# Performance work log

Measured on AMD Instinct MI355X. Metric: run time of the kernel, lower is better.

The kernel has to match this reference:

```python
import jax, jax.numpy as jnp
import numpy as np

MOMENTUM = 0.99
EPS = 1e-08


def setup_inputs() -> dict:
    key = jax.random.key(0)
    k1, = jax.random.split(key, 1)
    B, F, T = 32, 257, 3000
    mag = jax.random.uniform(k1, (B, F, T), dtype=jnp.float32)  # magnitudes >= 0
    bias = jnp.zeros((1,), dtype=jnp.float32)
    running_mean = jnp.ones((1,), dtype=jnp.float32)
    return {"mag": mag, "bias": bias, "running_mean": running_mean}


def reference(mag, bias, running_mean):
    """Causal per-frame EMA energy normalization (eval-mode sequence path).

    mag: [B, F, T] -> (mag_norm [B, F, T], mag_mean [B, 1, T])
    """
    B, F, T = mag.shape
    frame_means = mag.mean(axis=1)          # [B, T]
    init = jnp.broadcast_to(running_mean, (B,))  # m_0 = running_mean per batch

    def step(carry, fm_t):
        m = MOMENTUM * carry + (1.0 - MOMENTUM) * fm_t  # [B]
        return m, m

    _, means = jax.lax.scan(step, init, frame_means.T)  # means: [T, B]
    mean_with_bias = means.T + bias[0]                  # [B, T]
    mag_norm = mag / (mean_with_bias[:, None, :] + EPS)  # [B, F, T]
    mag_mean = mean_with_bias[:, None, :]               # [B, 1, T]
    return mag_norm, mag_mean
```

## Files before the change

kernel.cpp:

```cpp
#include <hip/hip_runtime.h>


#define B_  32
#define F_  257
#define T_  3000
#define CHUNKS 8
#define FCH 33
#define MOM 0.99f
#define OMM 0.01f
#define EPS_ 1e-8f

__global__ __launch_bounds__(256) void k1_partial(const float* __restrict__ mag,
                                                  float* __restrict__ part) {
    int g  = blockIdx.x * 256 + threadIdx.x;
    int tt = g % 750;
    int b  = (g / 750) % B_;
    int c  = g / (750 * B_);
    int f0 = c * FCH;
    int f1 = min(f0 + FCH, F_);
    const float4* magv = reinterpret_cast<const float4*>(mag);
    int base = (b * F_ + f0) * 750 + tt;
    float4 s = make_float4(0.f, 0.f, 0.f, 0.f);
    for (int f = f0; f < f1; ++f) {
        float4 v = magv[base];
        s.x += v.x; s.y += v.y; s.z += v.z; s.w += v.w;
        base += 750;
    }
    reinterpret_cast<float4*>(part)[(c * B_ + b) * 750 + tt] = s;
}

__global__ __launch_bounds__(256) void k2_scan(const float* __restrict__ part,
                                               const float* __restrict__ bias,
                                               const float* __restrict__ rmean,
                                               float* __restrict__ mag_mean,
                                               float* __restrict__ recip) {
    __shared__ float xs[T_];
    __shared__ float sA[256];
    __shared__ float sB[256];
    const int b = blockIdx.x;
    const int tid = threadIdx.x;

    for (int t = tid; t < T_; t += 256) {
        float s = 0.f;
        #pragma unroll
        for (int c = 0; c < CHUNKS; ++c) s += part[(c * B_ + b) * T_ + t];
        xs[t] = s * (1.0f / F_);
    }
    __syncthreads();

    const int CH = 12;
    const int t0 = tid * CH;
    float A = 1.f, Bv = 0.f;
    if (t0 < T_) {
        #pragma unroll
        for (int j = 0; j < CH; ++j) {
            float x = xs[t0 + j];
            Bv = MOM * Bv + OMM * x;
            A *= MOM;
        }
    }
    sA[tid] = A; sB[tid] = Bv;
    __syncthreads();

    for (int off = 1; off < 256; off <<= 1) {
        float cA = sA[tid], cB = sB[tid];
        float pA = 1.f, pB = 0.f;
        if (tid >= off) { pA = sA[tid - off]; pB = sB[tid - off]; }
        __syncthreads();
        if (tid >= off) { sA[tid] = pA * cA; sB[tid] = pB * cA + cB; }
        __syncthreads();
    }

    float pA = 1.f, pB = 0.f;
    if (tid > 0) { pA = sA[tid - 1]; pB = sB[tid - 1]; }

    if (t0 < T_) {
        float m = pA * rmean[0] + pB;
        float bias0 = bias[0];
        #pragma unroll
        for (int j = 0; j < CH; ++j) {
            float x = xs[t0 + j];
            m = MOM * m + OMM * x;
            float mb = m + bias0;
            mag_mean[b * T_ + t0 + j] = mb;
            recip[b * T_ + t0 + j] = 1.0f / (mb + EPS_);
        }
    }
}

__global__ __launch_bounds__(256) void k3_norm(const float* __restrict__ mag,
                                               const float* __restrict__ recip,
                                               float* __restrict__ out) {
    const int N4 = B_ * F_ * T_ / 4;
    int i4 = blockIdx.x * 256 + threadIdx.x;
    if (i4 >= N4) return;
    float4 v = reinterpret_cast<const float4*>(mag)[i4];
    int b  = i4 / (F_ * T_ / 4);
    int t4 = i4 % (T_ / 4);
    float4 r = reinterpret_cast<const float4*>(recip)[b * (T_ / 4) + t4];
    float4 o;
    o.x = v.x * r.x; o.y = v.y * r.y; o.z = v.z * r.z; o.w = v.w * r.w;
    reinterpret_cast<float4*>(out)[i4] = o;
}

extern "C" void kernel_launch(void* const* d_in, const int* in_sizes, int n_in,
                              void* d_out, int out_size, void* d_ws, size_t ws_size,
                              hipStream_t stream) {
    const float* mag   = (const float*)d_in[0];
    const float* bias  = (const float*)d_in[1];
    const float* rmean = (const float*)d_in[2];
    float* out      = (float*)d_out;
    float* mag_mean = out + (size_t)B_ * F_ * T_;
    float* part  = (float*)d_ws;
    float* recip = part + (size_t)CHUNKS * B_ * T_;

    k1_partial<<<CHUNKS * B_ * 750 / 256, 256, 0, stream>>>(mag, part);
    k2_scan<<<B_, 256, 0, stream>>>(part, bias, rmean, mag_mean, recip);
    const int N4 = B_ * F_ * T_ / 4;
    k3_norm<<<(N4 + 255) / 256, 256, 0, stream>>>(mag, recip, out);
}
```

Before: 199.7 us.

## Restructure reduction, scan output, and normalize kernels around whole-row blocks

The partial-sum kernel now gives each block one batch and one of 16 frequency chunks, and each thread covers up to three float4 columns across the row. This raises the chunk count and reduces the grid to 512 blocks. The scan kernel stages its results in shared memory and writes mag_mean and recip with coalesced strided stores instead of per-thread contiguous runs. The normalize kernel launches one block per (b,f) row, which removes the per-element division and modulo indexing. Fewer, larger blocks in the reduction may lower occupancy and memory-level parallelism.

```diff
diff --git a/kernel.cpp b/kernel.cpp
--- a/kernel.cpp
+++ b/kernel.cpp
@@ -4,29 +4,41 @@
 #define B_  32
 #define F_  257
 #define T_  3000
-#define CHUNKS 8
-#define FCH 33
+#define T4  750
+#define NCH 16
 #define MOM 0.99f
 #define OMM 0.01f
 #define EPS_ 1e-8f
 
-__global__ __launch_bounds__(256) void k1_partial(const float* __restrict__ mag,
-                                                  float* __restrict__ part) {
-    int g  = blockIdx.x * 256 + threadIdx.x;
-    int tt = g % 750;
-    int b  = (g / 750) % B_;
-    int c  = g / (750 * B_);
-    int f0 = c * FCH;
-    int f1 = min(f0 + FCH, F_);
+__global__ __launch_bounds__(256) void k1_rowsum(const float* __restrict__ mag,
+                                                 float* __restrict__ part) {
+    const int blk = blockIdx.x;
+    const int b   = blk >> 4;
+    const int c   = blk & (NCH - 1);
+    const int f0  = (c * F_) / NCH;
+    const int f1  = ((c + 1) * F_) / NCH;
+    const int tid = threadIdx.x;
     const float4* magv = reinterpret_cast<const float4*>(mag);
-    int base = (b * F_ + f0) * 750 + tt;
-    float4 s = make_float4(0.f, 0.f, 0.f, 0.f);
-    for (int f = f0; f < f1; ++f) {
-        float4 v = magv[base];
-        s.x += v.x; s.y += v.y; s.z += v.z; s.w += v.w;
-        base += 750;
+
+    float4 a0 = make_float4(0.f, 0.f, 0.f, 0.f);
+    float4 a1 = a0, a2 = a0;
+    const bool has2 = tid < (T4 - 512);
+
+    int base = (b * F_ + f0) * T4;
+    for (int f = f0; f < f1; ++f, base += T4) {
+        float4 v0 = magv[base + tid];
+        float4 v1 = magv[base + tid + 256];
+        a0.x += v0.x; a0.y += v0.y; a0.z += v0.z; a0.w += v0.w;
+        a1.x += v1.x; a1.y += v1.y; a1.z += v1.z; a1.w += v1.w;
+        if (has2) {
+            float4 v2 = magv[base + tid + 512];
+            a2.x += v2.x; a2.y += v2.y; a2.z += v2.z; a2.w += v2.w;
+        }
     }
-    reinterpret_cast<float4*>(part)[(c * B_ + b) * 750 + tt] = s;
+    float4* pv = reinterpret_cast<float4*>(part);
+    pv[blk * T4 + tid]       = a0;
+    pv[blk * T4 + tid + 256] = a1;
+    if (has2) pv[blk * T4 + tid + 512] = a2;
 }
 
 __global__ __launch_bounds__(256) void k2_scan(const float* __restrict__ part,
@@ -43,7 +55,7 @@
     for (int t = tid; t < T_; t += 256) {
         float s = 0.f;
         #pragma unroll
-        for (int c = 0; c < CHUNKS; ++c) s += part[(c * B_ + b) * T_ + t];
+        for (int c = 0; c < NCH; ++c) s += part[(b * NCH + c) * T_ + t];
         xs[t] = s * (1.0f / F_);
     }
     __syncthreads();
@@ -73,34 +85,54 @@
 
     float pA = 1.f, pB = 0.f;
     if (tid > 0) { pA = sA[tid - 1]; pB = sB[tid - 1]; }
+    __syncthreads();
 
+    const float bias0 = bias[0];
     if (t0 < T_) {
         float m = pA * rmean[0] + pB;
-        float bias0 = bias[0];
         #pragma unroll
         for (int j = 0; j < CH; ++j) {
             float x = xs[t0 + j];
             m = MOM * m + OMM * x;
-            float mb = m + bias0;
-            mag_mean[b * T_ + t0 + j] = mb;
-            recip[b * T_ + t0 + j] = 1.0f / (mb + EPS_);
+            xs[t0 + j] = m + bias0;
         }
+    }
+    __syncthreads();
+
+    for (int t = tid; t < T_; t += 256) {
+        float mb = xs[t];
+        mag_mean[b * T_ + t] = mb;
+        recip[b * T_ + t]    = 1.0f / (mb + EPS_);
     }
 }
 
 __global__ __launch_bounds__(256) void k3_norm(const float* __restrict__ mag,
                                                const float* __restrict__ recip,
                                                float* __restrict__ out) {
-    const int N4 = B_ * F_ * T_ / 4;
-    int i4 = blockIdx.x * 256 + threadIdx.x;
-    if (i4 >= N4) return;
-    float4 v = reinterpret_cast<const float4*>(mag)[i4];
-    int b  = i4 / (F_ * T_ / 4);
-    int t4 = i4 % (T_ / 4);
-    float4 r = reinterpret_cast<const float4*>(recip)[b * (T_ / 4) + t4];
+    const int r   = blockIdx.x;
+    const int b   = r / F_;
+    const int tid = threadIdx.x;
+    const float4* magv = reinterpret_cast<const float4*>(mag);
+    const float4* rv   = reinterpret_cast<const float4*>(recip);
+    float4* ov         = reinterpret_cast<float4*>(out);
+    const int base  = r * T4;
+    const int rbase = b * T4;
+
+    float4 v0 = magv[base + tid];
+    float4 r0 = rv[rbase + tid];
+    float4 v1 = magv[base + tid + 256];
+    float4 r1 = rv[rbase + tid + 256];
     float4 o;
-    o.x = v.x * r.x; o.y = v.y * r.y; o.z = v.z * r.z; o.w = v.w * r.w;
-    reinterpret_cast<float4*>(out)[i4] = o;
+    o.x = v0.x * r0.x; o.y = v0.y * r0.y; o.z = v0.z * r0.z; o.w = v0.w * r0.w;
+    ov[base + tid] = o;
+    o.x = v1.x * r1.x; o.y = v1.y * r1.y; o.z = v1.z * r1.z; o.w = v1.w * r1.w;
+    ov[base + tid + 256] = o;
+    if (tid < T4 - 512) {
+        float4 v2 = magv[base + tid + 512];
+        float4 r2 = rv[rbase + tid + 512];
+        o.x = v2.x * r2.x; o.y = v2.y * r2.y; o.z = v2.z * r2.z; o.w = v2.w * r2.w;
+        ov[base + tid + 512] = o;
+    }
 }
 
 extern "C" void kernel_launch(void* const* d_in, const int* in_sizes, int n_in,
@@ -112,10 +144,9 @@
     float* out      = (float*)d_out;
     float* mag_mean = out + (size_t)B_ * F_ * T_;
     float* part  = (float*)d_ws;
-    float* recip = part + (size_t)CHUNKS * B_ * T_;
+    float* recip = part + (size_t)B_ * NCH * T_;
 
-    k1_partial<<<CHUNKS * B_ * 750 / 256, 256, 0, stream>>>(mag, part);
+    k1_rowsum<<<B_ * NCH, 256, 0, stream>>>(mag, part);
     k2_scan<<<B_, 256, 0, stream>>>(part, bias, rmean, mag_mean, recip);
-    const int N4 = B_ * F_ * T_ / 4;
-    k3_norm<<<(N4 + 255) / 256, 256, 0, stream>>>(mag, recip, out);
+    k3_norm<<<B_ * F_, 256, 0, stream>>>(mag, recip, out);
 }
```

After: 203.9 us. +2.1%, slower.
